# Kernel tuning notes

Measured on AMD Instinct MI355X. Metric: run time of the kernel, lower is better.

## Reference

```python
import jax, jax.numpy as jnp
import numpy as np

B = 4096
P_HID = 1024
H_HID = 512
MAX_P = 128
MAX_HE = MAX_P // 3  # 42
TAU = 1.0
EPS = 1e-20


def setup_inputs() -> dict:
    key = jax.random.key(0)
    ks = jax.random.split(key, 12)
    s_p = 1.0 / np.sqrt(P_HID)
    s_h = 1.0 / np.sqrt(H_HID)
    # gumbel noise: g = -log(-log(U))
    u_p = jax.random.uniform(ks[3], (B, MAX_P, 2), minval=EPS, maxval=1.0)
    u_h = jax.random.uniform(ks[4], (B, MAX_HE, 2), minval=EPS, maxval=1.0)
    return {
        "particle_h": jax.random.normal(ks[0], (B, P_HID), jnp.float32),
        "edge_h": jax.random.normal(ks[1], (B, H_HID), jnp.float32),
        "hyperedge_h": jax.random.normal(ks[2], (B, H_HID), jnp.float32),
        "g_p": -jnp.log(-jnp.log(u_p)),
        "g_h": -jnp.log(-jnp.log(u_h)),
        "W1_p": jax.random.normal(ks[5], (P_HID, P_HID), jnp.float32) * s_p,
        "b1_p": jnp.zeros((P_HID,), jnp.float32),
        "W2_p": jax.random.normal(ks[6], (P_HID, MAX_P), jnp.float32) * s_p,
        "b2_p": jnp.zeros((MAX_P,), jnp.float32),
        "W1_h": jax.random.normal(ks[7], (H_HID, H_HID), jnp.float32) * s_h,
        "b1_h": jnp.zeros((H_HID,), jnp.float32),
        "W2_h": jax.random.normal(ks[8], (H_HID, MAX_HE), jnp.float32) * s_h,
        "b2_h": jnp.zeros((MAX_HE,), jnp.float32),
    }


def _gumbel_hard_st(logits, g, tau):
    """F.gumbel_softmax(stack([l,-l],-1), tau, hard=True)[...,0] (straight-through)."""
    y = jax.nn.softmax((jnp.stack([logits, -logits], axis=-1) + g) / tau, axis=-1)
    y0 = y[..., 0]
    hard0 = (y0 > y[..., 1]).astype(y0.dtype)
    return hard0 + y0 - jax.lax.stop_gradient(y0)


def _mlp(x, W1, b1, W2, b2):
    return jax.nn.gelu(x @ W1 + b1, approximate=False) @ W2 + b2


def reference(particle_h, edge_h, hyperedge_h, g_p, g_h,
              W1_p, b1_p, W2_p, b2_p, W1_h, b1_h, W2_h, b2_h):
    particle_logits = _mlp(particle_h, W1_p, b1_p, W2_p, b2_p)      # [B, MAX_P]
    particle_mask = _gumbel_hard_st(particle_logits, g_p, TAU)      # [B, MAX_P]
    n_particles = particle_mask.sum(axis=-1).astype(jnp.int32)      # [B]

    # Ragged edge lists as a fixed padded buffer: all C(MAX_P,2) lexicographic
    # pairs (same order as torch.combinations); pair (i,j), i<j, is valid for
    # batch b iff j < n_particles[b].
    ii, jj = jnp.triu_indices(MAX_P, k=1)
    edge_index = jnp.stack([ii, jj]).astype(jnp.int32)              # [2, E_max]
    edge_valid = jj[None, :] < n_particles[:, None]                 # [B, E_max] bool

    hyperedge_logits = _mlp(hyperedge_h, W1_h, b1_h, W2_h, b2_h)    # [B, MAX_HE]
    hyperedge_mask = _gumbel_hard_st(hyperedge_logits, g_h, TAU)
    n_hyperedges = hyperedge_mask.sum(axis=-1).astype(jnp.int32)

    return (particle_mask, n_particles, edge_index, edge_valid,
            hyperedge_mask, n_hyperedges)
```

## Files before the change

kernel.cpp:

```cpp
#include <hip/hip_runtime.h>
#include <hip/hip_bf16.h>
#include <math.h>

typedef __bf16 bf16_t;
typedef bf16_t bf16x8 __attribute__((ext_vector_type(8)));
typedef bf16_t bf16x4 __attribute__((ext_vector_type(4)));
typedef float f32x4 __attribute__((ext_vector_type(4)));
typedef int i32x4 __attribute__((ext_vector_type(4)));
typedef unsigned int u32;

#define B_SZ 4096
#define P_HID 1024
#define H_HID 512
#define MAX_P 128
#define MAX_HE 42
#define HE_PAD 128
#define E_MAX 8128
#define E_MAX4 2032

__device__ __forceinline__ void async_cp16(const bf16_t* g, bf16_t* l) {
    __builtin_amdgcn_global_load_lds(
        (const __attribute__((address_space(1))) u32*)g,
        (__attribute__((address_space(3))) u32*)l, 16, 0, 0);
}

__device__ __forceinline__ float gelu_exact(float v) {
    return 0.5f * v * (1.f + erff(v * 0.70710678118654752f));
}

struct GemmP {
    const bf16_t *Ahi, *Alo, *BThi, *BTlo;
    const float* bias;
    bf16_t *Chi, *Clo;
    int N, K, nx;
};

template<int BM>
__global__ __launch_bounds__(256, 3) void gemm_pack(GemmP P, GemmP H, int pBlocks)
{
    constexpr int BN = 128;
    constexpr int MT = BM / 32;
    constexpr int NT = 4;
    constexpr int OPS_A = BM / 16;
    constexpr int OPS_B = BN / 16;
    constexpr int NOPS = 2 * OPS_A + 2 * OPS_B;
    constexpr int TILE = NOPS * 16 * 32;

    __shared__ __align__(16) bf16_t smem[2 * TILE];

    const bool isP = (int)blockIdx.x < pBlocks;
    const GemmP& a = isP ? P : H;
    const int bid  = isP ? blockIdx.x : blockIdx.x - pBlocks;
    const int bn   = (bid % a.nx) * BN;
    const int bm   = (bid / a.nx) * BM;
    const int K    = a.K;

    const int tid  = threadIdx.x;
    const int lane = tid & 63;
    const int wid  = tid >> 6;
    const int wm   = wid & 1;
    const int wn   = wid >> 1;

    const int srow = lane >> 2;
    const int scol = (lane & 3) * 8;
    const int fr   = lane & 15;
    const int fq   = lane >> 4;

    f32x4 acc[MT][NT];
#pragma unroll
    for (int i = 0; i < MT; ++i)
#pragma unroll
        for (int j = 0; j < NT; ++j)
            acc[i][j] = (f32x4){0.f, 0.f, 0.f, 0.f};

    const bf16_t* const gA0 = a.Ahi  + (size_t)bm * K;
    const bf16_t* const gA1 = a.Alo  + (size_t)bm * K;
    const bf16_t* const gB0 = a.BThi + (size_t)bn * K;
    const bf16_t* const gB1 = a.BTlo + (size_t)bn * K;

    auto stage = [&](int buf, int kt) {
#pragma unroll
        for (int o = 0; o < NOPS; ++o) {
            if ((o & 3) != wid) continue;
            const bf16_t* gsrc;
            int q, sec;
            if (o < OPS_A)                  { q = o;                     gsrc = gA0; sec = 0; }
            else if (o < 2 * OPS_A)         { q = o - OPS_A;             gsrc = gA1; sec = BM * 32; }
            else if (o < 2 * OPS_A + OPS_B) { q = o - 2 * OPS_A;         gsrc = gB0; sec = 2 * BM * 32; }
            else                            { q = o - 2 * OPS_A - OPS_B; gsrc = gB1; sec = 2 * BM * 32 + BN * 32; }
            async_cp16(gsrc + (size_t)(q * 16 + srow) * K + kt + scol,
                       smem + buf * TILE + sec + q * 16 * 32);
        }
    };

    stage(0, 0);
    __syncthreads();
    int cur = 0;
    for (int kt = 0; kt < K; kt += 32) {
        if (kt + 32 < K) stage(cur ^ 1, kt + 32);

        const bf16_t* const Tb = smem + cur * TILE;
        bf16x8 ah[MT], al[MT];
#pragma unroll
        for (int i = 0; i < MT; ++i) {
            const int row = wm * (BM / 2) + i * 16 + fr;
            ah[i] = *(const bf16x8*)(Tb + row * 32 + fq * 8);
            al[i] = *(const bf16x8*)(Tb + BM * 32 + row * 32 + fq * 8);
        }
#pragma unroll
        for (int j = 0; j < NT; ++j) {
            const int row = wn * 64 + j * 16 + fr;
            const bf16x8 bh = *(const bf16x8*)(Tb + 2 * BM * 32 + row * 32 + fq * 8);
            const bf16x8 bl = *(const bf16x8*)(Tb + 2 * BM * 32 + BN * 32 + row * 32 + fq * 8);
#pragma unroll
            for (int i = 0; i < MT; ++i) {
                acc[i][j] = __builtin_amdgcn_mfma_f32_16x16x32_bf16(ah[i], bh, acc[i][j], 0, 0, 0);
                acc[i][j] = __builtin_amdgcn_mfma_f32_16x16x32_bf16(ah[i], bl, acc[i][j], 0, 0, 0);
                acc[i][j] = __builtin_amdgcn_mfma_f32_16x16x32_bf16(al[i], bh, acc[i][j], 0, 0, 0);
            }
        }
        __syncthreads();
        cur ^= 1;
    }

#pragma unroll
    for (int i = 0; i < MT; ++i)
#pragma unroll
        for (int j = 0; j < NT; ++j) {
            const int col  = bn + wn * 64 + j * 16 + fr;
            const int row0 = bm + wm * (BM / 2) + i * 16 + fq * 4;
            const float bj = a.bias[col];
#pragma unroll
            for (int r = 0; r < 4; ++r) {
                float v = gelu_exact(acc[i][j][r] + bj);
                bf16_t h = (bf16_t)v;
                bf16_t l = (bf16_t)(v - (float)h);
                const size_t off = (size_t)(row0 + r) * a.N + col;
                a.Chi[off] = h;
                a.Clo[off] = l;
            }
        }
}

struct PartP {
    const bf16_t *Ahi, *Alo, *BThi, *BTlo;
    float* part;
    int K;
};

__global__ __launch_bounds__(256, 4) void gemm_logit_part(PartP P, PartP H, int pBlocks)
{
    constexpr int SPLITS = 4;
    constexpr int BM = 32, BN = 128, NT = 4;
    constexpr int OPS_A = BM / 16;
    constexpr int OPS_B = BN / 16;
    constexpr int NOPS  = 2 * OPS_A + 2 * OPS_B;
    constexpr int TILE  = NOPS * 16 * 32;

    __shared__ __align__(16) bf16_t smem[2 * TILE];

    const bool isP = (int)blockIdx.x < pBlocks;
    const PartP& a = isP ? P : H;
    const int bid   = isP ? blockIdx.x : blockIdx.x - pBlocks;
    const int tile  = bid >> 2;
    const int split = bid & (SPLITS - 1);
    const int bm    = tile * BM;
    const int K     = a.K;
    const int Ksub  = K / SPLITS;
    const int k0    = split * Ksub;

    const int tid  = threadIdx.x;
    const int lane = tid & 63;
    const int wid  = tid >> 6;
    const int wm   = wid & 1;
    const int wn   = wid >> 1;

    const int srow = lane >> 2;
    const int scol = (lane & 3) * 8;
    const int fr   = lane & 15;
    const int fq   = lane >> 4;

    f32x4 acc[NT];
#pragma unroll
    for (int j = 0; j < NT; ++j) acc[j] = (f32x4){0.f, 0.f, 0.f, 0.f};

    const bf16_t* const gA0 = a.Ahi  + (size_t)bm * K + k0;
    const bf16_t* const gA1 = a.Alo  + (size_t)bm * K + k0;
    const bf16_t* const gB0 = a.BThi + k0;
    const bf16_t* const gB1 = a.BTlo + k0;

    auto stage = [&](int buf, int kt) {
#pragma unroll
        for (int o = 0; o < NOPS; ++o) {
            if ((o & 3) != wid) continue;
            const bf16_t* gsrc;
            int q, sec;
            if (o < OPS_A)                  { q = o;                     gsrc = gA0; sec = 0; }
            else if (o < 2 * OPS_A)         { q = o - OPS_A;             gsrc = gA1; sec = BM * 32; }
            else if (o < 2 * OPS_A + OPS_B) { q = o - 2 * OPS_A;         gsrc = gB0; sec = 2 * BM * 32; }
            else                            { q = o - 2 * OPS_A - OPS_B; gsrc = gB1; sec = 2 * BM * 32 + BN * 32; }
            async_cp16(gsrc + (size_t)(q * 16 + srow) * K + kt + scol,
                       smem + buf * TILE + sec + q * 16 * 32);
        }
    };

    stage(0, 0);
    __syncthreads();
    int cur = 0;
    for (int kt = 0; kt < Ksub; kt += 32) {
        if (kt + 32 < Ksub) stage(cur ^ 1, kt + 32);

        const bf16_t* const Tb = smem + cur * TILE;
        const int arow = wm * 16 + fr;
        const bf16x8 ah = *(const bf16x8*)(Tb + arow * 32 + fq * 8);
        const bf16x8 al = *(const bf16x8*)(Tb + BM * 32 + arow * 32 + fq * 8);
#pragma unroll
        for (int j = 0; j < NT; ++j) {
            const int brow = wn * 64 + j * 16 + fr;
            const bf16x8 bh = *(const bf16x8*)(Tb + 2 * BM * 32 + brow * 32 + fq * 8);
            const bf16x8 bl = *(const bf16x8*)(Tb + 2 * BM * 32 + BN * 32 + brow * 32 + fq * 8);
            acc[j] = __builtin_amdgcn_mfma_f32_16x16x32_bf16(ah, bh, acc[j], 0, 0, 0);
            acc[j] = __builtin_amdgcn_mfma_f32_16x16x32_bf16(ah, bl, acc[j], 0, 0, 0);
            acc[j] = __builtin_amdgcn_mfma_f32_16x16x32_bf16(al, bh, acc[j], 0, 0, 0);
        }
        __syncthreads();
        cur ^= 1;
    }

    float* const pt = a.part + ((size_t)tile * SPLITS + split) * (BM * BN);
#pragma unroll
    for (int j = 0; j < NT; ++j)
#pragma unroll
        for (int r = 0; r < 4; ++r) {
            const int row_l = wm * 16 + fq * 4 + r;
            const int col   = wn * 64 + j * 16 + fr;
            pt[row_l * BN + col] = acc[j][r];
        }
}

struct RedP {
    const float *part, *bias, *g;
    float *out_mask, *out_n;
    int *ws_n;
    int NV;
};

__global__ __launch_bounds__(256) void logit_reduce(RedP P, RedP H, int pBlocks)
{
    constexpr int RB = 16;
    const bool isP = (int)blockIdx.x < pBlocks;
    const RedP& a = isP ? P : H;
    const int blk  = isP ? blockIdx.x : blockIdx.x - pBlocks;
    const int tile = blk >> 1;
    const int half = blk & 1;
    const int bm   = tile * 32 + half * RB;

    const int tid = threadIdx.x;
    const int c0  = (tid & 31) * 4;
    const int r0  = tid >> 5;
    const int NV  = a.NV;
    const float* const base = a.part + (size_t)tile * 4 * 32 * 128;

    float s[2];
#pragma unroll
    for (int rr = 0; rr < 2; ++rr) {
        const int row_l = half * RB + rr * 8 + r0;
        f32x4 v = *(const f32x4*)(a.bias + c0);
#pragma unroll
        for (int sp = 0; sp < 4; ++sp)
            v += *(const f32x4*)(base + sp * 4096 + row_l * 128 + c0);
        const int grow = tile * 32 + row_l;
        float cnt = 0.f;
#pragma unroll
        for (int k = 0; k < 4; ++k) {
            const int col = c0 + k;
            if (col < NV) {
                const size_t idx = (size_t)grow * NV + col;
                const float g0 = a.g[2 * idx + 0];
                const float g1 = a.g[2 * idx + 1];
                const float m = ((v[k] + g0) > (g1 - v[k])) ? 1.f : 0.f;
                a.out_mask[idx] = m;
                cnt += m;
            }
        }
        s[rr] = cnt;
    }
#pragma unroll
    for (int rr = 0; rr < 2; ++rr) {
        float t = s[rr];
        t += __shfl_xor(t, 1, 32);
        t += __shfl_xor(t, 2, 32);
        t += __shfl_xor(t, 4, 32);
        t += __shfl_xor(t, 8, 32);
        t += __shfl_xor(t, 16, 32);
        if ((tid & 31) == 0) {
            const int grow = tile * 32 + half * RB + rr * 8 + r0;
            a.out_n[grow] = t;
            if (a.ws_n) a.ws_n[grow] = (int)t;
        }
    }
}

struct PrepArgs {
    const float *ph, *hh, *W1p, *W2p, *W1h, *W2h;
    bf16_t *pA_hi, *pA_lo, *hA_hi, *hA_lo;
    bf16_t *W1pT_hi, *W1pT_lo, *W2pT_hi, *W2pT_lo;
    bf16_t *W1hT_hi, *W1hT_lo, *W2hT_hi, *W2hT_lo;
    float *out_ei; int *ws_jj;
};

__device__ __forceinline__ void split4(const float* x, bf16_t* hi, bf16_t* lo, int i) {
    float4 v = ((const float4*)x)[i];
    float vv[4] = {v.x, v.y, v.z, v.w};
    bf16x4 h, l;
#pragma unroll
    for (int r = 0; r < 4; ++r) {
        bf16_t hh = (bf16_t)vv[r];
        h[r] = hh;
        l[r] = (bf16_t)(vv[r] - (float)hh);
    }
    ((bf16x4*)hi)[i] = h;
    ((bf16x4*)lo)[i] = l;
}

__device__ __forceinline__ void tsplit(
    const float* W, bf16_t* Thi, bf16_t* Tlo, int K, int N,
    int t, int nx, float (*sh)[33], int tid)
{
    const int n0 = (t % nx) * 32, k0 = (t / nx) * 32;
    const int tx = tid & 31, ty = tid >> 5;
    for (int r = ty; r < 32; r += 8) {
        const int n = n0 + tx;
        sh[r][tx] = (n < N) ? W[(size_t)(k0 + r) * N + n] : 0.f;
    }
    __syncthreads();
    for (int r = ty; r < 32; r += 8) {
        const float x = sh[tx][r];
        bf16_t h = (bf16_t)x;
        bf16_t l = (bf16_t)(x - (float)h);
        const size_t off = (size_t)(n0 + r) * K + k0 + tx;
        Thi[off] = h;
        Tlo[off] = l;
    }
}

__device__ __forceinline__ int tri_off(int i) { return (i * (255 - i)) >> 1; }

__global__ __launch_bounds__(256) void prep_all(PrepArgs a)
{
    __shared__ float sh[32][33];
    const int bid = blockIdx.x;
    const int tid = threadIdx.x;

    if (bid < 4096) {
        split4(a.ph, a.pA_hi, a.pA_lo, bid * 256 + tid);
    } else if (bid < 6144) {
        split4(a.hh, a.hA_hi, a.hA_lo, (bid - 4096) * 256 + tid);
    } else if (bid < 7168) {
        tsplit(a.W1p, a.W1pT_hi, a.W1pT_lo, P_HID, P_HID, bid - 6144, 32, sh, tid);
    } else if (bid < 7296) {
        tsplit(a.W2p, a.W2pT_hi, a.W2pT_lo, P_HID, MAX_P, bid - 7168, 4, sh, tid);
    } else if (bid < 7552) {
        tsplit(a.W1h, a.W1hT_hi, a.W1hT_lo, H_HID, H_HID, bid - 7296, 16, sh, tid);
    } else if (bid < 7616) {
        tsplit(a.W2h, a.W2hT_hi, a.W2hT_lo, H_HID, MAX_HE, bid - 7552, 4, sh, tid);
    } else {
        const int e = (bid - 7616) * 256 + tid;
        if (e < E_MAX) {
            int i = (int)((255.0 - sqrt(65025.0 - 8.0 * (double)e)) * 0.5);
            if (i < 0) i = 0;
            if (i > 126) i = 126;
            while (i > 0 && tri_off(i) > e) --i;
            while (i < 126 && tri_off(i + 1) <= e) ++i;
            const int j = i + 1 + (e - tri_off(i));
            a.out_ei[e] = (float)i;
            a.out_ei[E_MAX + e] = (float)j;
            a.ws_jj[e] = j;
        }
    }
}

__global__ __launch_bounds__(256) void edge_valid_kernel(
    const int* __restrict__ ws_jj, const int* __restrict__ ws_n,
    float* __restrict__ out)
{
    const int b   = blockIdx.x >> 1;
    const int seg = blockIdx.x & 1;
    const int n   = ws_n[b];
    const int base = seg * (E_MAX4 / 2);
    float* const orow = out + (size_t)b * E_MAX;
#pragma unroll
    for (int it = 0; it < 4; ++it) {
        const int q = base + it * 256 + threadIdx.x;
        if (q < base + E_MAX4 / 2) {
            const i32x4 j4 = ((const i32x4*)ws_jj)[q];
            f32x4 v;
            v.x = (j4.x < n) ? 1.f : 0.f;
            v.y = (j4.y < n) ? 1.f : 0.f;
            v.z = (j4.z < n) ? 1.f : 0.f;
            v.w = (j4.w < n) ? 1.f : 0.f;
            __builtin_nontemporal_store(v, &((f32x4*)orow)[q]);
        }
    }
}

extern "C" void kernel_launch(void* const* d_in, const int* in_sizes, int n_in,
                              void* d_out, int out_size, void* d_ws, size_t ws_size,
                              hipStream_t stream)
{
    const float* particle_h  = (const float*)d_in[0];
    const float* hyperedge_h = (const float*)d_in[2];
    const float* g_p  = (const float*)d_in[3];
    const float* g_h  = (const float*)d_in[4];
    const float* W1_p = (const float*)d_in[5];
    const float* b1_p = (const float*)d_in[6];
    const float* W2_p = (const float*)d_in[7];
    const float* b2_p = (const float*)d_in[8];
    const float* W1_h = (const float*)d_in[9];
    const float* b1_h = (const float*)d_in[10];
    const float* W2_h = (const float*)d_in[11];
    const float* b2_h = (const float*)d_in[12];

    float* out = (float*)d_out;
    float* out_pmask = out;
    float* out_np    = out_pmask + (size_t)B_SZ * MAX_P;
    float* out_ei    = out_np + B_SZ;
    float* out_ev    = out_ei + 2 * E_MAX;
    float* out_hmask = out_ev + (size_t)B_SZ * E_MAX;
    float* out_nh    = out_hmask + (size_t)B_SZ * MAX_HE;

    char* w = (char*)d_ws;
    bf16_t* pA_hi   = (bf16_t*)w;  w += (size_t)B_SZ * P_HID * 2;
    bf16_t* pA_lo   = (bf16_t*)w;  w += (size_t)B_SZ * P_HID * 2;
    bf16_t* hA_hi   = (bf16_t*)w;  w += (size_t)B_SZ * H_HID * 2;
    bf16_t* hA_lo   = (bf16_t*)w;  w += (size_t)B_SZ * H_HID * 2;
    bf16_t* hidp_hi = (bf16_t*)w;  w += (size_t)B_SZ * P_HID * 2;
    bf16_t* hidp_lo = (bf16_t*)w;  w += (size_t)B_SZ * P_HID * 2;
    bf16_t* hidh_hi = (bf16_t*)w;  w += (size_t)B_SZ * H_HID * 2;
    bf16_t* hidh_lo = (bf16_t*)w;  w += (size_t)B_SZ * H_HID * 2;
    bf16_t* W1pT_hi = (bf16_t*)w;  w += (size_t)P_HID * P_HID * 2;
    bf16_t* W1pT_lo = (bf16_t*)w;  w += (size_t)P_HID * P_HID * 2;
    bf16_t* W2pT_hi = (bf16_t*)w;  w += (size_t)MAX_P * P_HID * 2;
    bf16_t* W2pT_lo = (bf16_t*)w;  w += (size_t)MAX_P * P_HID * 2;
    bf16_t* W1hT_hi = (bf16_t*)w;  w += (size_t)H_HID * H_HID * 2;
    bf16_t* W1hT_lo = (bf16_t*)w;  w += (size_t)H_HID * H_HID * 2;
    bf16_t* W2hT_hi = (bf16_t*)w;  w += (size_t)HE_PAD * H_HID * 2;
    bf16_t* W2hT_lo = (bf16_t*)w;  w += (size_t)HE_PAD * H_HID * 2;
    int*    ws_np   = (int*)w;     w += B_SZ * 4;
    int*    ws_jj   = (int*)w;     w += E_MAX * 4;

    float* part_base = (float*)pA_hi;

    PrepArgs pa;
    pa.ph = particle_h; pa.hh = hyperedge_h;
    pa.W1p = W1_p; pa.W2p = W2_p; pa.W1h = W1_h; pa.W2h = W2_h;
    pa.pA_hi = pA_hi; pa.pA_lo = pA_lo; pa.hA_hi = hA_hi; pa.hA_lo = hA_lo;
    pa.W1pT_hi = W1pT_hi; pa.W1pT_lo = W1pT_lo;
    pa.W2pT_hi = W2pT_hi; pa.W2pT_lo = W2pT_lo;
    pa.W1hT_hi = W1hT_hi; pa.W1hT_lo = W1hT_lo;
    pa.W2hT_hi = W2hT_hi; pa.W2hT_lo = W2hT_lo;
    pa.out_ei = out_ei; pa.ws_jj = ws_jj;
    prep_all<<<7648, 256, 0, stream>>>(pa);

    {
        GemmP P = {}, H = {};
        P.Ahi = pA_hi;  P.Alo = pA_lo;  P.BThi = W1pT_hi; P.BTlo = W1pT_lo;
        P.bias = b1_p;  P.Chi = hidp_hi; P.Clo = hidp_lo;
        P.N = P_HID; P.K = P_HID; P.nx = P_HID / 128;
        H.Ahi = hA_hi;  H.Alo = hA_lo;  H.BThi = W1hT_hi; H.BTlo = W1hT_lo;
        H.bias = b1_h;  H.Chi = hidh_hi; H.Clo = hidh_lo;
        H.N = H_HID; H.K = H_HID; H.nx = H_HID / 128;
        const int pB = (B_SZ / 64) * P.nx;
        const int hB = (B_SZ / 64) * H.nx;
        gemm_pack<64><<<pB + hB, 256, 0, stream>>>(P, H, pB);
    }

    {
        PartP P = {}, H = {};
        P.Ahi = hidp_hi; P.Alo = hidp_lo; P.BThi = W2pT_hi; P.BTlo = W2pT_lo;
        P.part = part_base; P.K = P_HID;
        H.Ahi = hidh_hi; H.Alo = hidh_lo; H.BThi = W2hT_hi; H.BTlo = W2hT_lo;
        H.part = part_base + (size_t)128 * 4 * 32 * 128; H.K = H_HID;
        const int pB = (B_SZ / 32) * 4;
        const int hB = (B_SZ / 32) * 4;
        gemm_logit_part<<<pB + hB, 256, 0, stream>>>(P, H, pB);
    }

    {
        RedP P = {}, H = {};
        P.part = part_base; P.bias = b2_p; P.g = g_p;
        P.out_mask = out_pmask; P.out_n = out_np; P.ws_n = ws_np; P.NV = MAX_P;
        H.part = part_base + (size_t)128 * 4 * 32 * 128; H.bias = b2_h; H.g = g_h;
        H.out_mask = out_hmask; H.out_n = out_nh; H.ws_n = nullptr; H.NV = MAX_HE;
        const int pB = B_SZ / 16;
        const int hB = B_SZ / 16;
        logit_reduce<<<pB + hB, 256, 0, stream>>>(P, H, pB);
    }

    edge_valid_kernel<<<2 * B_SZ, 256, 0, stream>>>(ws_jj, ws_np, out_ev);
}
```

Before: 261.6 us.

## Fuse edge-valid writer into logit reduction and swizzle GEMM block order

The edge_valid kernel is removed and its work folded into the logit reduction. Each block now handles four rows, one row per wavefront, reduces the particle count in-wave, passes it through shared memory, and writes the corresponding edge_valid rows directly. This drops a kernel launch and the count round-trip through workspace. Separately, the first GEMM remaps block indices with a stride-8 swizzle to change which tiles run concurrently, presumably for cache or channel locality. In exchange, hyperedge blocks now sit idle during the edge-writing phase, and each block issues a longer, more serialized stream of stores.

```diff
diff --git a/kernel.cpp b/kernel.cpp
--- a/kernel.cpp
+++ b/kernel.cpp
@@ -50,7 +50,11 @@
 
     const bool isP = (int)blockIdx.x < pBlocks;
     const GemmP& a = isP ? P : H;
-    const int bid  = isP ? blockIdx.x : blockIdx.x - pBlocks;
+    int bid = isP ? blockIdx.x : blockIdx.x - pBlocks;
+    {
+        const int nb = isP ? pBlocks : (int)gridDim.x - pBlocks;
+        bid = (bid & 7) * (nb >> 3) + (bid >> 3);
+    }
     const int bn   = (bid % a.nx) * BN;
     const int bm   = (bid / a.nx) * BM;
     const int K    = a.K;
@@ -238,65 +242,77 @@
         }
 }
 
-struct RedP {
+struct RedEV {
     const float *part, *bias, *g;
     float *out_mask, *out_n;
-    int *ws_n;
+    const int* jj;
+    float* ev;
     int NV;
 };
 
-__global__ __launch_bounds__(256) void logit_reduce(RedP P, RedP H, int pBlocks)
-{
-    constexpr int RB = 16;
+__global__ __launch_bounds__(256) void logit_reduce_ev(RedEV P, RedEV H, int pBlocks)
+{
+    __shared__ int sn[4];
     const bool isP = (int)blockIdx.x < pBlocks;
-    const RedP& a = isP ? P : H;
+    const RedEV& a = isP ? P : H;
     const int blk  = isP ? blockIdx.x : blockIdx.x - pBlocks;
-    const int tile = blk >> 1;
-    const int half = blk & 1;
-    const int bm   = tile * 32 + half * RB;
-
-    const int tid = threadIdx.x;
-    const int c0  = (tid & 31) * 4;
-    const int r0  = tid >> 5;
-    const int NV  = a.NV;
-    const float* const base = a.part + (size_t)tile * 4 * 32 * 128;
-
-    float s[2];
-#pragma unroll
-    for (int rr = 0; rr < 2; ++rr) {
-        const int row_l = half * RB + rr * 8 + r0;
-        f32x4 v = *(const f32x4*)(a.bias + c0);
-#pragma unroll
-        for (int sp = 0; sp < 4; ++sp)
-            v += *(const f32x4*)(base + sp * 4096 + row_l * 128 + c0);
-        const int grow = tile * 32 + row_l;
-        float cnt = 0.f;
-#pragma unroll
-        for (int k = 0; k < 4; ++k) {
-            const int col = c0 + k;
-            if (col < NV) {
-                const size_t idx = (size_t)grow * NV + col;
-                const float g0 = a.g[2 * idx + 0];
-                const float g1 = a.g[2 * idx + 1];
-                const float m = ((v[k] + g0) > (g1 - v[k])) ? 1.f : 0.f;
-                a.out_mask[idx] = m;
-                cnt += m;
-            }
-        }
-        s[rr] = cnt;
-    }
-#pragma unroll
-    for (int rr = 0; rr < 2; ++rr) {
-        float t = s[rr];
-        t += __shfl_xor(t, 1, 32);
-        t += __shfl_xor(t, 2, 32);
-        t += __shfl_xor(t, 4, 32);
-        t += __shfl_xor(t, 8, 32);
-        t += __shfl_xor(t, 16, 32);
-        if ((tid & 31) == 0) {
-            const int grow = tile * 32 + half * RB + rr * 8 + r0;
-            a.out_n[grow] = t;
-            if (a.ws_n) a.ws_n[grow] = (int)t;
+    const int tid  = threadIdx.x;
+    const int wid  = tid >> 6;
+    const int lane = tid & 63;
+
+    const int grow  = blk * 4 + wid;
+    const int tile  = grow >> 5;
+    const int row_l = grow & 31;
+    const float* const base = a.part + ((size_t)tile * 4 * 32 + row_l) * 128;
+    const int c0 = lane * 2;
+    float v0 = a.bias[c0];
+    float v1 = a.bias[c0 + 1];
+#pragma unroll
+    for (int sp = 0; sp < 4; ++sp) {
+        const float* p = base + sp * 4096;
+        v0 += p[c0];
+        v1 += p[c0 + 1];
+    }
+    const int NV = a.NV;
+    float cnt = 0.f;
+#pragma unroll
+    for (int k = 0; k < 2; ++k) {
+        const int col = c0 + k;
+        const float v = k ? v1 : v0;
+        if (col < NV) {
+            const size_t idx = (size_t)grow * NV + col;
+            const float g0 = a.g[2 * idx + 0];
+            const float g1 = a.g[2 * idx + 1];
+            const float m = ((v + g0) > (g1 - v)) ? 1.f : 0.f;
+            a.out_mask[idx] = m;
+            cnt += m;
+        }
+    }
+    cnt += __shfl_xor(cnt, 1, 64);
+    cnt += __shfl_xor(cnt, 2, 64);
+    cnt += __shfl_xor(cnt, 4, 64);
+    cnt += __shfl_xor(cnt, 8, 64);
+    cnt += __shfl_xor(cnt, 16, 64);
+    cnt += __shfl_xor(cnt, 32, 64);
+    if (lane == 0) {
+        a.out_n[grow] = cnt;
+        sn[wid] = (int)cnt;
+    }
+    __syncthreads();
+
+    if (!a.ev) return;
+#pragma unroll
+    for (int rr = 0; rr < 4; ++rr) {
+        const int n = sn[rr];
+        float* const orow = a.ev + (size_t)(blk * 4 + rr) * E_MAX;
+        for (int q = tid; q < E_MAX4; q += 256) {
+            const i32x4 j4 = ((const i32x4*)a.jj)[q];
+            f32x4 v;
+            v.x = (j4.x < n) ? 1.f : 0.f;
+            v.y = (j4.y < n) ? 1.f : 0.f;
+            v.z = (j4.z < n) ? 1.f : 0.f;
+            v.w = (j4.w < n) ? 1.f : 0.f;
+            __builtin_nontemporal_store(v, &((f32x4*)orow)[q]);
         }
     }
 }
@@ -380,30 +396,6 @@
     }
 }
 
-__global__ __launch_bounds__(256) void edge_valid_kernel(
-    const int* __restrict__ ws_jj, const int* __restrict__ ws_n,
-    float* __restrict__ out)
-{
-    const int b   = blockIdx.x >> 1;
-    const int seg = blockIdx.x & 1;
-    const int n   = ws_n[b];
-    const int base = seg * (E_MAX4 / 2);
-    float* const orow = out + (size_t)b * E_MAX;
-#pragma unroll
-    for (int it = 0; it < 4; ++it) {
-        const int q = base + it * 256 + threadIdx.x;
-        if (q < base + E_MAX4 / 2) {
-            const i32x4 j4 = ((const i32x4*)ws_jj)[q];
-            f32x4 v;
-            v.x = (j4.x < n) ? 1.f : 0.f;
-            v.y = (j4.y < n) ? 1.f : 0.f;
-            v.z = (j4.z < n) ? 1.f : 0.f;
-            v.w = (j4.w < n) ? 1.f : 0.f;
-            __builtin_nontemporal_store(v, &((f32x4*)orow)[q]);
-        }
-    }
-}
-
 extern "C" void kernel_launch(void* const* d_in, const int* in_sizes, int n_in,
                               void* d_out, int out_size, void* d_ws, size_t ws_size,
                               hipStream_t stream)
@@ -446,7 +438,6 @@
     bf16_t* W1hT_lo = (bf16_t*)w;  w += (size_t)H_HID * H_HID * 2;
     bf16_t* W2hT_hi = (bf16_t*)w;  w += (size_t)HE_PAD * H_HID * 2;
     bf16_t* W2hT_lo = (bf16_t*)w;  w += (size_t)HE_PAD * H_HID * 2;
-    int*    ws_np   = (int*)w;     w += B_SZ * 4;
     int*    ws_jj   = (int*)w;     w += E_MAX * 4;
 
     float* part_base = (float*)pA_hi;
@@ -487,15 +478,15 @@
     }
 
     {
-        RedP P = {}, H = {};
+        RedEV P = {}, H = {};
         P.part = part_base; P.bias = b2_p; P.g = g_p;
-        P.out_mask = out_pmask; P.out_n = out_np; P.ws_n = ws_np; P.NV = MAX_P;
+        P.out_mask = out_pmask; P.out_n = out_np;
+        P.jj = ws_jj; P.ev = out_ev; P.NV = MAX_P;
         H.part = part_base + (size_t)128 * 4 * 32 * 128; H.bias = b2_h; H.g = g_h;
-        H.out_mask = out_hmask; H.out_n = out_nh; H.ws_n = nullptr; H.NV = MAX_HE;
-        const int pB = B_SZ / 16;
-        const int hB = B_SZ / 16;
-        logit_reduce<<<pB + hB, 256, 0, stream>>>(P, H, pB);
-    }
-
-    edge_valid_kernel<<<2 * B_SZ, 256, 0, stream>>>(ws_jj, ws_np, out_ev);
-}
+        H.out_mask = out_hmask; H.out_n = out_nh;
+        H.jj = nullptr; H.ev = nullptr; H.NV = MAX_HE;
+        const int pB = B_SZ / 4;
+        const int hB = B_SZ / 4;
+        logit_reduce_ev<<<pB + hB, 256, 0, stream>>>(P, H, pB);
+    }
+}
```

New measurement: 258.1 us. No clear change (-1.3%).
